# Kernel optimization log

Measured on AMD Instinct MI355X. Metric: run time of the kernel, lower is better.

Reference implementation:

```python
import jax, jax.numpy as jnp
import numpy as np

B, S, F, H, NL, T = 64, 512, 256, 512, 1, 96
HA = H // 8  # attention hidden size (scale_factor=8)


def _p(key, shape, scale=0.05):
    return jax.random.normal(key, shape, dtype=jnp.float32) * scale


def setup_inputs() -> dict:
    key = jax.random.key(0)
    ks = jax.random.split(key, 20)
    return {
        "input_seq": jax.random.normal(ks[0], (B, S, F), dtype=jnp.float32),
        "h0": jax.random.normal(ks[1], (B, H), dtype=jnp.float32),
        "c0": jax.random.normal(ks[2], (B, H), dtype=jnp.float32),
        # encoder LSTM (torch gate order i,f,g,o), combined bias b_ih+b_hh
        "W_ih_e": _p(ks[3], (4 * H, F)),
        "W_hh_e": _p(ks[4], (4 * H, H)),
        "b_e": _p(ks[5], (4 * H,)),
        # decoder LSTM
        "W_ih_d": _p(ks[6], (4 * H, F)),
        "W_hh_d": _p(ks[7], (4 * H, H)),
        "b_d": _p(ks[8], (4 * H,)),
        # attention
        "We_p": _p(ks[9], (HA, H)),
        "be_p": _p(ks[10], (HA,)),
        "Wh_p": _p(ks[11], (HA, H)),
        "bh_p": _p(ks[12], (HA,)),
        "Wa": _p(ks[13], (HA, 2 * HA)),
        "ba": _p(ks[14], (HA,)),
        "v": jax.random.uniform(ks[15], (HA,), dtype=jnp.float32),
        # output linear: (H + HA) -> F
        "Wo": _p(ks[16], (F, H + HA)),
        "bo": _p(ks[17], (F,)),
        "output_size": T,
    }


def _lstm_step(x, h, c, Wih, Whh, b):
    gates = x @ Wih.T + h @ Whh.T + b  # (B, 4H)
    i, f, g, o = jnp.split(gates, 4, axis=-1)
    i, f, o = jax.nn.sigmoid(i), jax.nn.sigmoid(f), jax.nn.sigmoid(o)
    c = f * c + i * jnp.tanh(g)
    h = o * jnp.tanh(c)
    return h, c


def reference(input_seq, h0, c0, W_ih_e, W_hh_e, b_e, W_ih_d, W_hh_d, b_d,
              We_p, be_p, Wh_p, bh_p, Wa, ba, v, Wo, bo, output_size):
    # ---- encoder LSTM over seq (time-major scan) ----
    xs = jnp.swapaxes(input_seq, 0, 1)  # (S, B, F)

    def enc_step(carry, x):
        h, c = carry
        h, c = _lstm_step(x, h, c, W_ih_e, W_hh_e, b_e)
        return (h, c), h

    (h, c), enc_hs = jax.lax.scan(enc_step, (h0, c0), xs)
    enc_out = jnp.swapaxes(enc_hs, 0, 1)  # (B, S, H)

    # encoder projection (same every decode step; hoisted)
    enc_proj = enc_out @ We_p.T + be_p  # (B, S, HA)
    # split attn Linear weight: first HA cols act on hidden, last HA on enc_proj
    Wa_h, Wa_e = Wa[:, :HA], Wa[:, HA:]
    enc_attn = enc_proj @ Wa_e.T  # (B, S, HA)

    def dec_step(carry, _):
        x, h, c = carry
        # Bahdanau attention (uses pre-LSTM hidden h, per original)
        hq = h @ Wh_p.T + bh_p  # (B, HA)
        energy = jnp.tanh(hq[:, None, :] @ Wa_h.T + enc_attn + ba)  # (B, S, HA)
        scores = jnp.einsum('bsh,h->bs', energy, v)
        aw = jax.nn.softmax(scores, axis=1)  # (B, S)
        ctx = jnp.einsum('bs,bsh->bh', aw, enc_proj)  # (B, HA)
        # single-step decoder LSTM
        h, c = _lstm_step(x, h, c, W_ih_d, W_hh_d, b_d)
        out = jnp.concatenate([h, ctx], axis=1) @ Wo.T + bo  # (B, F)
        return (out, h, c), out

    carry0 = (input_seq[:, -1, :], h, c)
    _, preds = jax.lax.scan(dec_step, carry0, None, length=output_size)  # (T, B, F)
    # outputs[:, :, t] = pred_t; return outputs[:, -1, :] -> last feature over time
    return preds[:, :, -1].T  # (B, T)
```

## Files before the change

kernel.cpp:

```cpp
#include <hip/hip_runtime.h>


namespace {

__device__ __forceinline__ float fsigmoid(float x) {
    return 1.0f / (1.0f + __expf(-x));
}
__device__ __forceinline__ float ftanh(float x) {
    float e = __expf(2.0f * x);
    return 1.0f - 2.0f / (e + 1.0f);
}

__device__ __forceinline__ void coh_store(float* p, float v) {
    __hip_atomic_store(p, v, __ATOMIC_RELAXED, __HIP_MEMORY_SCOPE_AGENT);
}
__device__ __forceinline__ void coh_store2(float* p, float2 v) {
    union { float2 f; unsigned long long u; } cv; cv.f = v;
    __hip_atomic_store((unsigned long long*)p, cv.u,
                       __ATOMIC_RELAXED, __HIP_MEMORY_SCOPE_AGENT);
}

__device__ __forceinline__ void post_flag_rep(unsigned* flags, int stride,
                                              int idx, unsigned val) {
    if (threadIdx.x == 0) {
        asm volatile("s_waitcnt vmcnt(0)" ::: "memory");
        #pragma unroll
        for (int r = 0; r < 8; ++r)
            __hip_atomic_store(&flags[r * stride + idx], val,
                               __ATOMIC_RELAXED, __HIP_MEMORY_SCOPE_AGENT);
    }
}
__device__ __forceinline__ void wait_group(const unsigned* flags, int base,
                                           int mask, unsigned val) {
    const unsigned* f = flags + base + (threadIdx.x & mask);
    for (;;) {
        unsigned x = __hip_atomic_load(f, __ATOMIC_RELAXED, __HIP_MEMORY_SCOPE_AGENT);
        if (__all(x >= val)) break;
        __builtin_amdgcn_s_sleep(1);
    }
    asm volatile("" ::: "memory");
}
__device__ __forceinline__ void wait_lstm_inputs(const unsigned* attnF,
                                                 const unsigned* lstmF,
                                                 int w, unsigned val) {
    int lane = threadIdx.x & 63;
    const unsigned* fa = attnF + lane * 2;
    const unsigned* fl = lstmF + (w & 3) * 32 + (lane & 31);
    for (;;) {
        unsigned a = __hip_atomic_load(fa + 0, __ATOMIC_RELAXED, __HIP_MEMORY_SCOPE_AGENT);
        unsigned b = __hip_atomic_load(fa + 1, __ATOMIC_RELAXED, __HIP_MEMORY_SCOPE_AGENT);
        unsigned c = __hip_atomic_load(fl,     __ATOMIC_RELAXED, __HIP_MEMORY_SCOPE_AGENT);
        int ok = (a >= val) && (b >= val) && (c >= val);
        if (__all(ok)) break;
        __builtin_amdgcn_s_sleep(1);
    }
    asm volatile("" ::: "memory");
}

__global__ __launch_bounds__(256) void k_transpose_input(
    const float* __restrict__ in, float4* __restrict__ xQ)
{
    __shared__ float tile[64][65];
    int s  = blockIdx.x >> 2;
    int f0 = (blockIdx.x & 3) * 64;
    int lane = threadIdx.x & 63;
    int r0   = threadIdx.x >> 6;
    for (int r = r0; r < 64; r += 4)
        tile[r][lane] = in[(size_t)r * (512 * 256) + s * 256 + f0 + lane];
    __syncthreads();
    for (int q = r0; q < 16; q += 4) {
        float4 vv = make_float4(tile[lane][4*q], tile[lane][4*q+1],
                                tile[lane][4*q+2], tile[lane][4*q+3]);
        xQ[((size_t)s * 64 + (f0 >> 2) + q) * 64 + lane] = vv;
    }
}

__global__ __launch_bounds__(256) void k_prep(
    const float* __restrict__ We_p, const float* __restrict__ Wh_p,
    const float* __restrict__ h0,   const float* __restrict__ c0,
    const float* __restrict__ Wa,
    float* __restrict__ We_pT, float* __restrict__ Wh_pT,
    float* __restrict__ encH0, float* __restrict__ cT,
    float* __restrict__ WahT,  float* __restrict__ WaeT)
{
    int idx = blockIdx.x * blockDim.x + threadIdx.x;
    const int total = 32768 * 4 + 4096 * 2;
    for (; idx < total; idx += gridDim.x * blockDim.x) {
        if (idx < 32768) {
            int u = idx >> 6, h = idx & 63;
            We_pT[idx] = We_p[h * 512 + u];
        } else if (idx < 65536) {
            int i2 = idx - 32768; int k = i2 >> 6, i = i2 & 63;
            Wh_pT[i2] = Wh_p[i * 512 + k];
        } else if (idx < 98304) {
            int i2 = idx - 65536; int u = i2 >> 6, b = i2 & 63;
            encH0[(u >> 2) * 256 + b * 4 + (u & 3)] = h0[b * 512 + u];
        } else if (idx < 131072) {
            int i2 = idx - 98304; int u = i2 >> 6, b = i2 & 63;
            cT[i2] = c0[b * 512 + u];
        } else if (idx < 135168) {
            int i2 = idx - 131072; int j = i2 >> 6, i = i2 & 63;
            WahT[i2] = Wa[i * 128 + j];
        } else {
            int i2 = idx - 135168; int h2 = i2 >> 6, h = i2 & 63;
            WaeT[i2] = Wa[h * 128 + 64 + h2];
        }
    }
}

__global__ __launch_bounds__(256) void k_prep_wcomb(
    const float* __restrict__ Wih, const float* __restrict__ Whh,
    const float* __restrict__ Wo,  const float* __restrict__ bd,
    const float* __restrict__ bo,
    float* __restrict__ Wh, float* __restrict__ Wc, float* __restrict__ bprime)
{
    int r = blockIdx.x;
    for (int j = threadIdx.x; j < 576; j += 256) {
        float acc = 0.f;
        for (int f = 0; f < 256; ++f)
            acc = fmaf(Wih[r * 256 + f], Wo[f * 576 + j], acc);
        if (j < 512) Wh[(size_t)r * 512 + j] = acc + Whh[(size_t)r * 512 + j];
        else         Wc[(size_t)r * 64 + (j - 512)] = acc;
    }
    if (threadIdx.x == 0) {
        float s = bd[r];
        for (int f = 0; f < 256; ++f)
            s = fmaf(Wih[r * 256 + f], bo[f], s);
        bprime[r] = s;
    }
}

__global__ __launch_bounds__(256) void k_prep_g0(
    const float4* __restrict__ xQlast, const float* __restrict__ Wih,
    const float* __restrict__ bd, float* __restrict__ g0)
{
    int r = blockIdx.x * 4 + ((int)threadIdx.x >> 6);
    int lane = threadIdx.x & 63;
    const float4* Wih4 = (const float4*)Wih;
    float acc = bd[r];
    for (int q = 0; q < 64; ++q) {
        float4 a  = xQlast[q * 64 + lane];
        float4 wv = Wih4[(size_t)r * 64 + q];
        acc = fmaf(a.x, wv.x, acc); acc = fmaf(a.y, wv.y, acc);
        acc = fmaf(a.z, wv.z, acc); acc = fmaf(a.w, wv.w, acc);
    }
    g0[(size_t)r * 64 + lane] = acc;
}

template<int NQ>
__device__ __forceinline__ void accum_seg_pf(
    float acc[8], const float4* __restrict__ actQ, int qb,
    const float4* __restrict__ W4, int wstride, int u0, int lane)
{
    float4 a[NQ];
    #pragma unroll
    for (int q = 0; q < NQ; ++q)
        a[q] = actQ[(qb + q) * 64 + lane];
    #pragma unroll
    for (int q = 0; q < NQ; ++q) {
        #pragma unroll
        for (int uu = 0; uu < 2; ++uu)
            #pragma unroll
            for (int g = 0; g < 4; ++g) {
                float4 wv = W4[(size_t)(g * 512 + u0 + uu) * wstride + (qb + q)];
                float& A = acc[uu * 4 + g];
                A = fmaf(a[q].x, wv.x, A); A = fmaf(a[q].y, wv.y, A);
                A = fmaf(a[q].z, wv.z, A); A = fmaf(a[q].w, wv.w, A);
            }
    }
}

template<int NQ>
__device__ __forceinline__ void accum_seg_pf2(
    float accA[8], float accB[8], const float4* __restrict__ actQ, int qb,
    const float4* __restrict__ W4, int wstride, int u0A, int u0B, int lane)
{
    float4 a[NQ];
    #pragma unroll
    for (int q = 0; q < NQ; ++q)
        a[q] = actQ[(qb + q) * 64 + lane];
    #pragma unroll
    for (int q = 0; q < NQ; ++q) {
        #pragma unroll
        for (int uu = 0; uu < 2; ++uu)
            #pragma unroll
            for (int g = 0; g < 4; ++g) {
                float4 wA = W4[(size_t)(g * 512 + u0A + uu) * wstride + (qb + q)];
                float4 wB = W4[(size_t)(g * 512 + u0B + uu) * wstride + (qb + q)];
                float& A = accA[uu * 4 + g];
                float& Bv = accB[uu * 4 + g];
                A = fmaf(a[q].x, wA.x, A); A = fmaf(a[q].y, wA.y, A);
                A = fmaf(a[q].z, wA.z, A); A = fmaf(a[q].w, wA.w, A);
                Bv = fmaf(a[q].x, wB.x, Bv); Bv = fmaf(a[q].y, wB.y, Bv);
                Bv = fmaf(a[q].z, wB.z, Bv); Bv = fmaf(a[q].w, wB.w, Bv);
            }
    }
}

__device__ __forceinline__ void accum_ctx_reg(
    float acc[8], float4 c0, float4 c1,
    const float4* __restrict__ Wc4, int u0, int w)
{
    #pragma unroll
    for (int uu = 0; uu < 2; ++uu)
        #pragma unroll
        for (int g = 0; g < 4; ++g) {
            float4 w0 = Wc4[(size_t)(g * 512 + u0 + uu) * 16 + w * 2 + 0];
            float4 w1 = Wc4[(size_t)(g * 512 + u0 + uu) * 16 + w * 2 + 1];
            float& A = acc[uu * 4 + g];
            A = fmaf(c0.x, w0.x, A); A = fmaf(c0.y, w0.y, A);
            A = fmaf(c0.z, w0.z, A); A = fmaf(c0.w, w0.w, A);
            A = fmaf(c1.x, w1.x, A); A = fmaf(c1.y, w1.y, A);
            A = fmaf(c1.z, w1.z, A); A = fmaf(c1.w, w1.w, A);
        }
}

__device__ __forceinline__ void lstm_finish_vec(
    int u0, int tid, int w, float acc[8], float2& creg,
    const float* __restrict__ addVec, float* __restrict__ houtSlot, float* smem)
{
    int lane = tid & 63;
    float* part = smem;
    float* gsum = smem + 4096;
    #pragma unroll
    for (int r = 0; r < 8; ++r)
        part[(w * 8 + r) * 64 + lane] = acc[r];
    __syncthreads();
    {
        int b = tid & 63, r = tid >> 6;
        float s = 0.f;
        #pragma unroll
        for (int ww = 0; ww < 8; ++ww)
            s += part[(ww * 8 + r) * 64 + b];
        gsum[r * 64 + b] = s;
    }
    __syncthreads();
    if (tid < 64) {
        int b = tid;
        float cc[2] = {creg.x, creg.y};
        float hv[2];
        #pragma unroll
        for (int uu = 0; uu < 2; ++uu) {
            int u = u0 + uu;
            float gi = gsum[(uu*4+0)*64 + b] + addVec[u];
            float gf = gsum[(uu*4+1)*64 + b] + addVec[512 + u];
            float gg = gsum[(uu*4+2)*64 + b] + addVec[1024 + u];
            float go = gsum[(uu*4+3)*64 + b] + addVec[1536 + u];
            float si = fsigmoid(gi), sf = fsigmoid(gf), so = fsigmoid(go);
            float tg = ftanh(gg);
            float cn = sf * cc[uu] + si * tg;
            cc[uu] = cn;
            hv[uu] = so * ftanh(cn);
        }
        creg = make_float2(cc[0], cc[1]);
        coh_store2(houtSlot + (u0 >> 2) * 256 + b * 4 + (u0 & 3),
                   make_float2(hv[0], hv[1]));
    }
}

template<bool ROWADD>
__device__ __forceinline__ void lstm_finish2(
    int u0A, int u0B, int tid, int w, float accA[8], float accB[8],
    float2& creg, const float* __restrict__ addVec,
    const float* __restrict__ addRowB,
    float* __restrict__ houtSlot, float* smem)
{
    int lane = tid & 63;
    float* part = smem;
    #pragma unroll
    for (int r = 0; r < 8; ++r)
        part[(w * 16 + r) * 64 + lane] = accA[r];
    #pragma unroll
    for (int r = 0; r < 8; ++r)
        part[(w * 16 + 8 + r) * 64 + lane] = accB[r];
    __syncthreads();
    if (tid < 128) {
        int b  = tid & 63;
        int ps = tid >> 6;
        int u0 = ps ? u0B : u0A;
        float cc[2] = {creg.x, creg.y};
        float hv[2];
        #pragma unroll
        for (int uu = 0; uu < 2; ++uu) {
            int u = u0 + uu;
            float gate[4];
            #pragma unroll
            for (int g = 0; g < 4; ++g) {
                int row = ps * 8 + uu * 4 + g;
                float s = 0.f;
                #pragma unroll
                for (int ww = 0; ww < 8; ++ww)
                    s += part[(ww * 16 + row) * 64 + b];
                if (ROWADD) s += addRowB[(size_t)(g * 512 + u) * 64 + b];
                else        s += addVec[g * 512 + u];
                gate[g] = s;
            }
            float si = fsigmoid(gate[0]), sf = fsigmoid(gate[1]);
            float so = fsigmoid(gate[3]);
            float tg = ftanh(gate[2]);
            float cn = sf * cc[uu] + si * tg;
            cc[uu] = cn;
            hv[uu] = so * ftanh(cn);
        }
        creg = make_float2(cc[0], cc[1]);
        coh_store2(houtSlot + (u0 >> 2) * 256 + b * 4 + (u0 & 3),
                   make_float2(hv[0], hv[1]));
        asm volatile("s_waitcnt vmcnt(0)" ::: "memory");
    }
    __syncthreads();
}

__global__ __launch_bounds__(512, 2) void k_enc_persistent(
    const float4* __restrict__ xQ, float* __restrict__ encH,
    float* __restrict__ cT,
    const float* __restrict__ Wih, const float* __restrict__ Whh,
    const float* __restrict__ bias, unsigned* flagsR)
{
    __shared__ float smem[4608];
    int tid = threadIdx.x;
    int lane = tid & 63;
    int w = __builtin_amdgcn_readfirstlane(tid >> 6);
    int bi = blockIdx.x;
    int u0 = bi * 2;
    const unsigned* myFlags = flagsR + (bi & 7) * 256;
    const float4* Wih4 = (const float4*)Wih;
    const float4* Whh4 = (const float4*)Whh;
    float2 creg = make_float2(0.f, 0.f);
    if (tid < 64) { creg.x = cT[u0 * 64 + tid]; creg.y = cT[(u0 + 1) * 64 + tid]; }
    float acc[8];
    #pragma unroll
    for (int r = 0; r < 8; ++r) acc[r] = 0.f;
    accum_seg_pf<8>(acc, xQ, w * 8, Wih4, 64, u0, lane);
    for (int t = 0; t < 512; ++t) {
        wait_group(myFlags, w * 32, 31, (unsigned)t);
        accum_seg_pf<16>(acc, (const float4*)(encH + (size_t)t * 32768),
                         w * 16, Whh4, 128, u0, lane);
        lstm_finish_vec(u0, tid, w, acc, creg, bias,
                        encH + (size_t)(t + 1) * 32768, smem);
        post_flag_rep(flagsR, 256, bi, (unsigned)(t + 1));
        #pragma unroll
        for (int r = 0; r < 8; ++r) acc[r] = 0.f;
        if (t + 1 < 512)
            accum_seg_pf<8>(acc, xQ + (size_t)(t + 1) * 4096, w * 8, Wih4, 64, u0, lane);
    }
    if (tid < 64) { cT[u0 * 64 + tid] = creg.x; cT[(u0 + 1) * 64 + tid] = creg.y; }
}

__global__ __launch_bounds__(256) void k_proj_attn(
    const float* __restrict__ encH,  const float* __restrict__ We_pT,
    const float* __restrict__ be_p,  const float* __restrict__ WaeT,
    const float* __restrict__ ba,
    float* __restrict__ encProj, float* __restrict__ attnPre)
{
    int lane = threadIdx.x & 63;
    int w    = __builtin_amdgcn_readfirstlane((int)threadIdx.x >> 6);
    int wid  = blockIdx.x * 4 + w;
    int b    = wid >> 6;
    int soct = wid & 63;
    float acc[8];
    float bep = be_p[lane];
    #pragma unroll
    for (int j = 0; j < 8; ++j) acc[j] = bep;
    #pragma unroll 2
    for (int q = 0; q < 128; ++q) {
        float w0 = We_pT[(4*q+0) * 64 + lane];
        float w1 = We_pT[(4*q+1) * 64 + lane];
        float w2 = We_pT[(4*q+2) * 64 + lane];
        float w3 = We_pT[(4*q+3) * 64 + lane];
        #pragma unroll
        for (int j = 0; j < 8; ++j) {
            const float4* hb4 = (const float4*)(encH + (size_t)(soct*8 + j + 1) * 32768);
            float4 hv = hb4[q * 64 + b];
            acc[j] = fmaf(hv.x, w0, acc[j]); acc[j] = fmaf(hv.y, w1, acc[j]);
            acc[j] = fmaf(hv.z, w2, acc[j]); acc[j] = fmaf(hv.w, w3, acc[j]);
        }
    }
    #pragma unroll
    for (int j = 0; j < 8; ++j)
        encProj[((size_t)b * 512 + soct * 8 + j) * 64 + lane] = acc[j];
    #pragma unroll
    for (int j = 0; j < 8; ++j) {
        float aa = ba[lane];
        for (int h2 = 0; h2 < 64; ++h2)
            aa = fmaf(__shfl(acc[j], h2), WaeT[h2 * 64 + lane], aa);
        attnPre[((size_t)b * 512 + soct * 8 + j) * 64 + lane] = aa;
    }
}

__global__ __launch_bounds__(256) void k_attn_transpose(
    const float* __restrict__ attnPre, float* __restrict__ attnPreT)
{
    __shared__ float tile[64][65];
    int b  = blockIdx.x >> 3;
    int s0 = (blockIdx.x & 7) * 64;
    int lane = threadIdx.x & 63;
    int r0   = threadIdx.x >> 6;
    for (int r = r0; r < 64; r += 4)
        tile[r][lane] = attnPre[(size_t)b * 32768 + (size_t)(s0 + r) * 64 + lane];
    __syncthreads();
    for (int r = r0; r < 64; r += 4)
        attnPreT[(size_t)b * 32768 + (size_t)r * 512 + s0 + lane] = tile[lane][r];
}

__device__ __forceinline__ void attention_half(
    int b, int tid, int w, int lane,
    const float* __restrict__ hcur,
    const float* __restrict__ Wh_pT, const float* __restrict__ bh_p,
    const float* __restrict__ WahT,  const float* __restrict__ v,
    const float* __restrict__ apL,
    const float* __restrict__ epL,
    float* __restrict__ ctxsumOut,
    float* __restrict__ mSOut,
    float* smem)
{
    float* hq  = smem;
    float* hWa = smem + 64;
    float* sc  = smem + 128;
    float* part = smem + 384;
    float* red  = smem + 896;
    {
        const float4* h4 = (const float4*)hcur;
        float4 hv[16];
        #pragma unroll
        for (int j = 0; j < 16; ++j)
            hv[j] = h4[(w * 16 + j) * 64 + b];
        float p = 0.f;
        #pragma unroll
        for (int j = 0; j < 16; ++j) {
            int q = w * 16 + j;
            p = fmaf(hv[j].x, Wh_pT[(4*q+0) * 64 + lane], p);
            p = fmaf(hv[j].y, Wh_pT[(4*q+1) * 64 + lane], p);
            p = fmaf(hv[j].z, Wh_pT[(4*q+2) * 64 + lane], p);
            p = fmaf(hv[j].w, Wh_pT[(4*q+3) * 64 + lane], p);
        }
        part[w * 64 + lane] = p;
    }
    __syncthreads();
    if (tid < 64) {
        float s = bh_p[tid];
        #pragma unroll
        for (int ww = 0; ww < 8; ++ww) s += part[ww * 64 + tid];
        hq[tid] = s;
    }
    __syncthreads();
    if (tid < 64) {
        float s = 0.f;
        for (int j = 0; j < 64; ++j)
            s = fmaf(hq[j], WahT[j * 64 + tid], s);
        hWa[tid] = s;
    }
    __syncthreads();
    {
        int sp  = tid & 255;
        int hh0 = (tid >> 8) * 32;
        float acc = 0.f;
        for (int j = 0; j < 32; ++j) {
            int h = hh0 + j;
            float e = ftanh(hWa[h] + apL[h * 256 + sp]);
            acc = fmaf(v[h], e, acc);
        }
        part[tid] = acc;
    }
    __syncthreads();
    if (tid < 256)
        sc[tid] = part[tid] + part[256 + tid];
    __syncthreads();
    if (tid < 256) {
        float x = sc[tid];
        float m = x;
        #pragma unroll
        for (int off = 32; off > 0; off >>= 1)
            m = fmaxf(m, __shfl_xor(m, off));
        if (lane == 0) red[w] = m;
    }
    __syncthreads();
    if (tid == 0)
        red[8] = fmaxf(fmaxf(red[0], red[1]), fmaxf(red[2], red[3]));
    __syncthreads();
    float M = red[8];
    if (tid < 256) {
        float e = __expf(sc[tid] - M);
        sc[tid] = e;
        float s = e;
        #pragma unroll
        for (int off = 32; off > 0; off >>= 1)
            s += __shfl_xor(s, off);
        if (lane == 0) red[w] = s;
    }
    __syncthreads();
    if (tid == 0)
        red[9] = ((red[0] + red[1]) + (red[2] + red[3]));
    __syncthreads();
    {
        float a = 0.f;
        for (int i = 0; i < 32; ++i) {
            int sp2 = w * 32 + i;
            a = fmaf(sc[sp2], epL[sp2 * 64 + lane], a);
        }
        part[w * 64 + lane] = a;
    }
    __syncthreads();
    if (tid < 64) {
        float s = 0.f;
        #pragma unroll
        for (int ww = 0; ww < 8; ++ww) s += part[ww * 64 + tid];
        coh_store(&ctxsumOut[(tid >> 2) * 256 + b * 4 + (tid & 3)], s);
    }
    if (tid == 0) {
        coh_store(&mSOut[b], M);
        coh_store(&mSOut[64 + b], red[9]);
    }
    __syncthreads();
}

__device__ __forceinline__ void load_ctx_quads(
    int t, int w, int lane,
    const float* __restrict__ ctxsumH, const float* __restrict__ mSbuf,
    float4& c0, float4& c1)
{
    const float* mS = mSbuf + (size_t)(t - 1) * 256;
    float m0 = mS[lane],       S0 = mS[64 + lane];
    float m1 = mS[128 + lane], S1 = mS[192 + lane];
    float M  = fmaxf(m0, m1);
    float e0 = __expf(m0 - M), e1 = __expf(m1 - M);
    float inv = 1.0f / (e0 * S0 + e1 * S1);
    e0 *= inv; e1 *= inv;
    const float4* a0 = (const float4*)(ctxsumH + (size_t)(t - 1) * 8192);
    const float4* a1 = (const float4*)(ctxsumH + (size_t)(t - 1) * 8192 + 4096);
    float4 x0 = a0[(w * 2 + 0) * 64 + lane];
    float4 y0 = a1[(w * 2 + 0) * 64 + lane];
    float4 x1 = a0[(w * 2 + 1) * 64 + lane];
    float4 y1 = a1[(w * 2 + 1) * 64 + lane];
    c0 = make_float4(e0 * x0.x + e1 * y0.x, e0 * x0.y + e1 * y0.y,
                     e0 * x0.z + e1 * y0.z, e0 * x0.w + e1 * y0.w);
    c1 = make_float4(e0 * x1.x + e1 * y1.x, e0 * x1.y + e1 * y1.y,
                     e0 * x1.z + e1 * y1.z, e0 * x1.w + e1 * y1.w);
}

extern __shared__ float dynsmem[];
__global__ __launch_bounds__(512) void k_dec_persistent(
    const float* __restrict__ encHend,
    float* __restrict__ dechH,
    float* __restrict__ cT,
    const float* __restrict__ Whh,
    const float* __restrict__ Wh,
    const float* __restrict__ Wc,
    const float* __restrict__ g0, const float* __restrict__ bprime,
    const float* __restrict__ Wh_pT, const float* __restrict__ bh_p,
    const float* __restrict__ WahT,  const float* __restrict__ v,
    const float* __restrict__ attnPreT, const float* __restrict__ encProj,
    float* __restrict__ ctxsumH,
    float* __restrict__ mSbuf,
    unsigned* attnFlagsR, unsigned* lstmFlagsR)
{
    float* smem = dynsmem;
    float* apL  = dynsmem + 4608;
    float* epL  = apL + 16384;
    int tid = threadIdx.x;
    int lane = tid & 63;
    int w = __builtin_amdgcn_readfirstlane(tid >> 6);
    int bi = blockIdx.x;
    int rep = bi & 7;
    const unsigned* myLstmF = lstmFlagsR + rep * 128;
    const unsigned* myAttnF = attnFlagsR + rep * 128;
    if (bi < 128) {
        int b = bi & 63, half = bi >> 6;
        {
            const float4* src = (const float4*)(attnPreT + (size_t)b * 32768 + half * 256);
            float4* dst = (float4*)apL;
            for (int i = tid; i < 4096; i += 512) {
                int h = i >> 6, qc = i & 63;
                dst[i] = src[(size_t)h * 128 + qc];
            }
        }
        {
            const float4* src = (const float4*)(encProj + ((size_t)b * 512 + half * 256) * 64);
            float4* dst = (float4*)epL;
            for (int i = tid; i < 4096; i += 512)
                dst[i] = src[i];
        }
        __syncthreads();
        for (int t = 0; t < 96; ++t) {
            if (t) wait_group(myLstmF, (w & 3) * 32, 31, (unsigned)t);
            const float* hc = t ? dechH + (size_t)(t - 1) * 32768 : encHend;
            attention_half(b, tid, w, lane, hc, Wh_pT, bh_p, WahT, v,
                           apL, epL,
                           ctxsumH + (size_t)t * 8192 + half * 4096,
                           mSbuf + (size_t)t * 256 + half * 128, smem);
            post_flag_rep(attnFlagsR, 128, bi, (unsigned)(t + 1));
        }
    } else {
        int u0A = (bi - 128) * 2;
        int u0B = u0A + 256;
        const float4* Whh4 = (const float4*)Whh;
        const float4* Wh4  = (const float4*)Wh;
        const float4* Wc4  = (const float4*)Wc;
        float2 creg = make_float2(0.f, 0.f);
        if (tid < 64) {
            creg.x = cT[u0A * 64 + tid]; creg.y = cT[(u0A + 1) * 64 + tid];
        } else if (tid < 128) {
            creg.x = cT[u0B * 64 + (tid - 64)];
            creg.y = cT[(u0B + 1) * 64 + (tid - 64)];
        }
        for (int t = 0; t < 96; ++t) {
            if (t) wait_lstm_inputs(myAttnF, myLstmF, w, (unsigned)t);
            const float* hc = t ? dechH + (size_t)(t - 1) * 32768 : encHend;
            float* hn = dechH + (size_t)t * 32768;
            float accA[8], accB[8];
            #pragma unroll
            for (int r = 0; r < 8; ++r) { accA[r] = 0.f; accB[r] = 0.f; }
            if (t == 0) {
                accum_seg_pf2<16>(accA, accB, (const float4*)hc, w * 16,
                                  Whh4, 128, u0A, u0B, lane);
                lstm_finish2<true>(u0A, u0B, tid, w, accA, accB, creg,
                                   nullptr, g0, hn, smem);
            } else {
                float4 cq0, cq1;
                load_ctx_quads(t, w, lane, ctxsumH, mSbuf, cq0, cq1);
                accum_seg_pf2<16>(accA, accB, (const float4*)hc, w * 16,
                                  Wh4, 128, u0A, u0B, lane);
                accum_ctx_reg(accA, cq0, cq1, Wc4, u0A, w);
                accum_ctx_reg(accB, cq0, cq1, Wc4, u0B, w);
                lstm_finish2<false>(u0A, u0B, tid, w, accA, accB, creg,
                                    bprime, nullptr, hn, smem);
            }
            post_flag_rep(lstmFlagsR, 128, bi - 128, (unsigned)(t + 1));
        }
    }
}

__global__ __launch_bounds__(256) void k_dout(
    const float* __restrict__ dechH,
    const float* __restrict__ ctxsumH, const float* __restrict__ mSbuf,
    const float* __restrict__ Wo, const float* __restrict__ bo,
    float* __restrict__ dout)
{
    __shared__ float part[256];
    int tau = blockIdx.x;
    int tid = threadIdx.x;
    int lane = tid & 63;
    int w = tid >> 6;
    const float* hq = dechH + (size_t)tau * 32768;
    const float* wrow = Wo + 255 * 576;
    float acc = 0.f;
    for (int i = w * 128; i < w * 128 + 128; ++i)
        acc = fmaf(wrow[i], hq[(i >> 2) * 256 + lane * 4 + (i & 3)], acc);
    part[w * 64 + lane] = acc;
    __syncthreads();
    if (tid < 64) {
        int b = tid;
        const float* mS = mSbuf + (size_t)tau * 256;
        float m0 = mS[b],       S0 = mS[64 + b];
        float m1 = mS[128 + b], S1 = mS[192 + b];
        float M  = fmaxf(m0, m1);
        float e0 = __expf(m0 - M), e1 = __expf(m1 - M);
        float inv = 1.0f / (e0 * S0 + e1 * S1);
        e0 *= inv; e1 *= inv;
        const float* cs0 = ctxsumH + (size_t)tau * 8192;
        const float* cs1 = cs0 + 4096;
        float a2 = bo[255];
        for (int h2 = 0; h2 < 64; ++h2) {
            int idx = (h2 >> 2) * 256 + b * 4 + (h2 & 3);
            a2 = fmaf(wrow[512 + h2], e0 * cs0[idx] + e1 * cs1[idx], a2);
        }
        float s = a2 + part[b] + part[64 + b] + part[128 + b] + part[192 + b];
        dout[b * 96 + tau] = s;
    }
}

}

extern "C" void kernel_launch(void* const* d_in, const int* in_sizes, int n_in,
                              void* d_out, int out_size, void* d_ws, size_t ws_size,
                              hipStream_t stream)
{
    (void)in_sizes; (void)n_in; (void)out_size; (void)ws_size;
    const float* input_seq = (const float*)d_in[0];
    const float* h0     = (const float*)d_in[1];
    const float* c0     = (const float*)d_in[2];
    const float* W_ih_e = (const float*)d_in[3];
    const float* W_hh_e = (const float*)d_in[4];
    const float* b_e    = (const float*)d_in[5];
    const float* W_ih_d = (const float*)d_in[6];
    const float* W_hh_d = (const float*)d_in[7];
    const float* b_d    = (const float*)d_in[8];
    const float* We_p   = (const float*)d_in[9];
    const float* be_p   = (const float*)d_in[10];
    const float* Wh_p   = (const float*)d_in[11];
    const float* bh_p   = (const float*)d_in[12];
    const float* Wa     = (const float*)d_in[13];
    const float* ba     = (const float*)d_in[14];
    const float* v      = (const float*)d_in[15];
    const float* Wo     = (const float*)d_in[16];
    const float* bo     = (const float*)d_in[17];
    float* out = (float*)d_out;

    unsigned* encFlagsR  = (unsigned*)d_ws;
    unsigned* attnFlagsR = encFlagsR + 2048;
    unsigned* lstmFlagsR = attnFlagsR + 1024;
    float* ws       = (float*)d_ws + 4096;
    float* xT       = ws;
    float* encH     = xT + 8388608;
    float* cT       = encH + 16809984;
    float* We_pT    = cT + 32768;
    float* Wh_pT    = We_pT + 32768;
    float* WahT     = Wh_pT + 32768;
    float* WaeT     = WahT + 4096;
    float* encProj  = WaeT + 4096;
    float* attnPre  = encProj + 2097152;
    float* dechH    = attnPre + 2097152;
    float* ctxsumH  = dechH + 3145728;
    float* mSbuf    = ctxsumH + 786432;
    float* Wh       = mSbuf + 24576;
    float* Wc       = Wh + 1048576;
    float* bprime   = Wc + 131072;
    float* g0       = bprime + 2048;
    float* attnPreT = xT;

    (void)hipFuncSetAttribute((const void*)k_dec_persistent,
                              hipFuncAttributeMaxDynamicSharedMemorySize, 149504);

    (void)hipMemsetAsync(d_ws, 0, 16384, stream);
    k_transpose_input<<<2048, 256, 0, stream>>>(input_seq, (float4*)xT);
    k_prep<<<544, 256, 0, stream>>>(We_p, Wh_p, h0, c0, Wa,
                                    We_pT, Wh_pT, encH, cT, WahT, WaeT);
    k_prep_wcomb<<<2048, 256, 0, stream>>>(W_ih_d, W_hh_d, Wo, b_d, bo,
                                           Wh, Wc, bprime);
    k_prep_g0<<<512, 256, 0, stream>>>((const float4*)(xT + (size_t)511 * 16384),
                                       W_ih_d, b_d, g0);
    k_enc_persistent<<<256, 512, 0, stream>>>((const float4*)xT, encH, cT,
                                              W_ih_e, W_hh_e, b_e, encFlagsR);
    k_proj_attn<<<1024, 256, 0, stream>>>(encH, We_pT, be_p, WaeT, ba,
                                          encProj, attnPre);
    k_attn_transpose<<<512, 256, 0, stream>>>(attnPre, attnPreT);
    k_dec_persistent<<<256, 512, 149504, stream>>>(encH + (size_t)512 * 32768,
                                                   dechH, cT,
                                                   W_hh_d, Wh, Wc, g0, bprime,
                                                   Wh_pT, bh_p, WahT, v,
                                                   attnPreT, encProj,
                                                   ctxsumH, mSbuf,
                                                   attnFlagsR, lstmFlagsR);
    k_dout<<<96, 256, 0, stream>>>(dechH, ctxsumH, mSbuf, Wo, bo, out);
}
```

Before: 5.226 ms.

## Replace encoder step flags with sentinel-polled hidden-state data

The encoder's per-step flag wait and flag post are removed. Instead, each wave polls the hidden-state slab directly with atomic loads until the values differ from a sentinel pattern that a new memset writes over the whole encH buffer beforehand. This removes one flag round-trip per timestep and lets each wave start as soon as its own slice is written, rather than waiting for a group of blocks. In exchange it adds a 64 MB memset, polling traffic on the data itself, and relies on a computed value never equalling the sentinel bits.

```diff
diff --git a/kernel.cpp b/kernel.cpp
--- a/kernel.cpp
+++ b/kernel.cpp
@@ -2,6 +2,8 @@
 
 
 namespace {
+
+#define H_SENTINEL 0x7F7F7F7Fu
 
 __device__ __forceinline__ float fsigmoid(float x) {
     return 1.0f / (1.0f + __expf(-x));
@@ -170,6 +172,52 @@
     }
 }
 
+__device__ __forceinline__ void accum_h_poll(
+    float acc[8], const float* __restrict__ hslab, int w,
+    const float4* __restrict__ W4, int u0, int lane)
+{
+    const unsigned long long* hp = (const unsigned long long*)hslab;
+    #pragma unroll
+    for (int jg = 0; jg < 4; ++jg) {
+        unsigned long long uv[8];
+        unsigned pend = 0xFFu;
+        for (;;) {
+            #pragma unroll
+            for (int i = 0; i < 8; ++i) {
+                if (pend & (1u << i)) {
+                    int q = w * 16 + jg * 4 + (i >> 1);
+                    unsigned long long x = __hip_atomic_load(
+                        &hp[(size_t)q * 128 + lane * 2 + (i & 1)],
+                        __ATOMIC_RELAXED, __HIP_MEMORY_SCOPE_AGENT);
+                    if ((unsigned)x != H_SENTINEL) {
+                        uv[i] = x;
+                        pend &= ~(1u << i);
+                    }
+                }
+            }
+            if (__all(pend == 0)) break;
+            __builtin_amdgcn_s_sleep(1);
+        }
+        asm volatile("" ::: "memory");
+        #pragma unroll
+        for (int j = 0; j < 4; ++j) {
+            int q = jg * 4 + j;
+            union { unsigned long long u; float2 f; } lo, hi;
+            lo.u = uv[2 * j]; hi.u = uv[2 * j + 1];
+            float ax = lo.f.x, ay = lo.f.y, az = hi.f.x, aw = hi.f.y;
+            #pragma unroll
+            for (int uu = 0; uu < 2; ++uu)
+                #pragma unroll
+                for (int g = 0; g < 4; ++g) {
+                    float4 wv = W4[(size_t)(g * 512 + u0 + uu) * 128 + (w * 16 + q)];
+                    float& A = acc[uu * 4 + g];
+                    A = fmaf(ax, wv.x, A); A = fmaf(ay, wv.y, A);
+                    A = fmaf(az, wv.z, A); A = fmaf(aw, wv.w, A);
+                }
+        }
+    }
+}
+
 template<int NQ>
 __device__ __forceinline__ void accum_seg_pf2(
     float accA[8], float accB[8], const float4* __restrict__ actQ, int qb,
@@ -314,7 +362,7 @@
     const float4* __restrict__ xQ, float* __restrict__ encH,
     float* __restrict__ cT,
     const float* __restrict__ Wih, const float* __restrict__ Whh,
-    const float* __restrict__ bias, unsigned* flagsR)
+    const float* __restrict__ bias)
 {
     __shared__ float smem[4608];
     int tid = threadIdx.x;
@@ -322,7 +370,6 @@
     int w = __builtin_amdgcn_readfirstlane(tid >> 6);
     int bi = blockIdx.x;
     int u0 = bi * 2;
-    const unsigned* myFlags = flagsR + (bi & 7) * 256;
     const float4* Wih4 = (const float4*)Wih;
     const float4* Whh4 = (const float4*)Whh;
     float2 creg = make_float2(0.f, 0.f);
@@ -332,12 +379,9 @@
     for (int r = 0; r < 8; ++r) acc[r] = 0.f;
     accum_seg_pf<8>(acc, xQ, w * 8, Wih4, 64, u0, lane);
     for (int t = 0; t < 512; ++t) {
-        wait_group(myFlags, w * 32, 31, (unsigned)t);
-        accum_seg_pf<16>(acc, (const float4*)(encH + (size_t)t * 32768),
-                         w * 16, Whh4, 128, u0, lane);
+        accum_h_poll(acc, encH + (size_t)t * 32768, w, Whh4, u0, lane);
         lstm_finish_vec(u0, tid, w, acc, creg, bias,
                         encH + (size_t)(t + 1) * 32768, smem);
-        post_flag_rep(flagsR, 256, bi, (unsigned)(t + 1));
         #pragma unroll
         for (int r = 0; r < 8; ++r) acc[r] = 0.f;
         if (t + 1 < 512)
@@ -695,8 +739,7 @@
     const float* bo     = (const float*)d_in[17];
     float* out = (float*)d_out;
 
-    unsigned* encFlagsR  = (unsigned*)d_ws;
-    unsigned* attnFlagsR = encFlagsR + 2048;
+    unsigned* attnFlagsR = (unsigned*)d_ws;
     unsigned* lstmFlagsR = attnFlagsR + 1024;
     float* ws       = (float*)d_ws + 4096;
     float* xT       = ws;
@@ -721,6 +764,7 @@
                               hipFuncAttributeMaxDynamicSharedMemorySize, 149504);
 
     (void)hipMemsetAsync(d_ws, 0, 16384, stream);
+    (void)hipMemsetAsync(encH + 32768, 0x7F, (size_t)512 * 32768 * 4, stream);
     k_transpose_input<<<2048, 256, 0, stream>>>(input_seq, (float4*)xT);
     k_prep<<<544, 256, 0, stream>>>(We_p, Wh_p, h0, c0, Wa,
                                     We_pT, Wh_pT, encH, cT, WahT, WaeT);
@@ -729,7 +773,7 @@
     k_prep_g0<<<512, 256, 0, stream>>>((const float4*)(xT + (size_t)511 * 16384),
                                        W_ih_d, b_d, g0);
     k_enc_persistent<<<256, 512, 0, stream>>>((const float4*)xT, encH, cT,
-                                              W_ih_e, W_hh_e, b_e, encFlagsR);
+                                              W_ih_e, W_hh_e, b_e);
     k_proj_attn<<<1024, 256, 0, stream>>>(encH, We_pT, be_p, WaeT, ba,
                                           encProj, attnPre);
     k_attn_transpose<<<512, 256, 0, stream>>>(attnPre, attnPreT);
```

Result: slower. 9.361 ms (+79.1%).

## Fold decoder weight-combine and g0 prep into encoder persistent kernel slack

Applied to the files above, without the earlier changes.

Removes the separate k_prep_wcomb and k_prep_g0 launches. Their work is spread across the first 16 timesteps of the persistent encoder kernel: each block computes 8 combined-weight rows and 8 g0 rows, placed after it posts its step flag. This is meant to hide the prep work in the idle time while blocks wait on inter-block flags, and to save two launches. The risk is that the extra work sits on the serial recurrence's critical path in those early steps and delays other blocks waiting on the flags. The g0 path also adds extra __syncthreads and shared-memory scratch use.

```diff
diff --git a/kernel.cpp b/kernel.cpp
--- a/kernel.cpp
+++ b/kernel.cpp
@@ -108,45 +108,6 @@
     }
 }
 
-__global__ __launch_bounds__(256) void k_prep_wcomb(
-    const float* __restrict__ Wih, const float* __restrict__ Whh,
-    const float* __restrict__ Wo,  const float* __restrict__ bd,
-    const float* __restrict__ bo,
-    float* __restrict__ Wh, float* __restrict__ Wc, float* __restrict__ bprime)
-{
-    int r = blockIdx.x;
-    for (int j = threadIdx.x; j < 576; j += 256) {
-        float acc = 0.f;
-        for (int f = 0; f < 256; ++f)
-            acc = fmaf(Wih[r * 256 + f], Wo[f * 576 + j], acc);
-        if (j < 512) Wh[(size_t)r * 512 + j] = acc + Whh[(size_t)r * 512 + j];
-        else         Wc[(size_t)r * 64 + (j - 512)] = acc;
-    }
-    if (threadIdx.x == 0) {
-        float s = bd[r];
-        for (int f = 0; f < 256; ++f)
-            s = fmaf(Wih[r * 256 + f], bo[f], s);
-        bprime[r] = s;
-    }
-}
-
-__global__ __launch_bounds__(256) void k_prep_g0(
-    const float4* __restrict__ xQlast, const float* __restrict__ Wih,
-    const float* __restrict__ bd, float* __restrict__ g0)
-{
-    int r = blockIdx.x * 4 + ((int)threadIdx.x >> 6);
-    int lane = threadIdx.x & 63;
-    const float4* Wih4 = (const float4*)Wih;
-    float acc = bd[r];
-    for (int q = 0; q < 64; ++q) {
-        float4 a  = xQlast[q * 64 + lane];
-        float4 wv = Wih4[(size_t)r * 64 + q];
-        acc = fmaf(a.x, wv.x, acc); acc = fmaf(a.y, wv.y, acc);
-        acc = fmaf(a.z, wv.z, acc); acc = fmaf(a.w, wv.w, acc);
-    }
-    g0[(size_t)r * 64 + lane] = acc;
-}
-
 template<int NQ>
 __device__ __forceinline__ void accum_seg_pf(
     float acc[8], const float4* __restrict__ actQ, int qb,
@@ -310,11 +271,65 @@
     __syncthreads();
 }
 
+__device__ __forceinline__ void wcomb_row(
+    int r, int tid,
+    const float* __restrict__ WihD, const float* __restrict__ WhhD,
+    const float* __restrict__ Wo,   const float* __restrict__ bd,
+    const float* __restrict__ bo,
+    float* __restrict__ Wh, float* __restrict__ Wc, float* __restrict__ bprime)
+{
+    for (int j = tid; j < 576; j += 512) {
+        float acc = 0.f;
+        for (int f = 0; f < 256; ++f)
+            acc = fmaf(WihD[r * 256 + f], Wo[f * 576 + j], acc);
+        if (j < 512) Wh[(size_t)r * 512 + j] = acc + WhhD[(size_t)r * 512 + j];
+        else         Wc[(size_t)r * 64 + (j - 512)] = acc;
+    }
+    if (tid == 0) {
+        float s = bd[r];
+        for (int f = 0; f < 256; ++f)
+            s = fmaf(WihD[r * 256 + f], bo[f], s);
+        bprime[r] = s;
+    }
+}
+
+__device__ __forceinline__ void g0_row(
+    int r, int tid, int w, int lane,
+    const float4* __restrict__ xQlast, const float* __restrict__ WihD,
+    const float* __restrict__ bd, float* __restrict__ g0, float* smem)
+{
+    const float4* Wih4 = (const float4*)WihD;
+    float acc = 0.f;
+    #pragma unroll
+    for (int j = 0; j < 8; ++j) {
+        int q = w * 8 + j;
+        float4 a  = xQlast[q * 64 + lane];
+        float4 wv = Wih4[(size_t)r * 64 + q];
+        acc = fmaf(a.x, wv.x, acc); acc = fmaf(a.y, wv.y, acc);
+        acc = fmaf(a.z, wv.z, acc); acc = fmaf(a.w, wv.w, acc);
+    }
+    float* scratch = smem + 4096;
+    __syncthreads();
+    scratch[w * 64 + lane] = acc;
+    __syncthreads();
+    if (tid < 64) {
+        float s = bd[r];
+        #pragma unroll
+        for (int ww = 0; ww < 8; ++ww) s += scratch[ww * 64 + tid];
+        g0[(size_t)r * 64 + tid] = s;
+    }
+}
+
 __global__ __launch_bounds__(512, 2) void k_enc_persistent(
     const float4* __restrict__ xQ, float* __restrict__ encH,
     float* __restrict__ cT,
     const float* __restrict__ Wih, const float* __restrict__ Whh,
-    const float* __restrict__ bias, unsigned* flagsR)
+    const float* __restrict__ bias, unsigned* flagsR,
+    const float* __restrict__ WihD, const float* __restrict__ WhhD,
+    const float* __restrict__ Wo,   const float* __restrict__ bd,
+    const float* __restrict__ bo,
+    float* __restrict__ Wh, float* __restrict__ Wc,
+    float* __restrict__ bprime, float* __restrict__ g0)
 {
     __shared__ float smem[4608];
     int tid = threadIdx.x;
@@ -325,6 +340,7 @@
     const unsigned* myFlags = flagsR + (bi & 7) * 256;
     const float4* Wih4 = (const float4*)Wih;
     const float4* Whh4 = (const float4*)Whh;
+    const float4* xQlast = xQ + (size_t)511 * 4096;
     float2 creg = make_float2(0.f, 0.f);
     if (tid < 64) { creg.x = cT[u0 * 64 + tid]; creg.y = cT[(u0 + 1) * 64 + tid]; }
     float acc[8];
@@ -338,6 +354,10 @@
         lstm_finish_vec(u0, tid, w, acc, creg, bias,
                         encH + (size_t)(t + 1) * 32768, smem);
         post_flag_rep(flagsR, 256, bi, (unsigned)(t + 1));
+        if (t < 8)
+            wcomb_row(bi * 8 + t, tid, WihD, WhhD, Wo, bd, bo, Wh, Wc, bprime);
+        else if (t < 16)
+            g0_row(bi * 8 + (t - 8), tid, w, lane, xQlast, WihD, bd, g0, smem);
         #pragma unroll
         for (int r = 0; r < 8; ++r) acc[r] = 0.f;
         if (t + 1 < 512)
@@ -724,12 +744,10 @@
     k_transpose_input<<<2048, 256, 0, stream>>>(input_seq, (float4*)xT);
     k_prep<<<544, 256, 0, stream>>>(We_p, Wh_p, h0, c0, Wa,
                                     We_pT, Wh_pT, encH, cT, WahT, WaeT);
-    k_prep_wcomb<<<2048, 256, 0, stream>>>(W_ih_d, W_hh_d, Wo, b_d, bo,
-                                           Wh, Wc, bprime);
-    k_prep_g0<<<512, 256, 0, stream>>>((const float4*)(xT + (size_t)511 * 16384),
-                                       W_ih_d, b_d, g0);
     k_enc_persistent<<<256, 512, 0, stream>>>((const float4*)xT, encH, cT,
-                                              W_ih_e, W_hh_e, b_e, encFlagsR);
+                                              W_ih_e, W_hh_e, b_e, encFlagsR,
+                                              W_ih_d, W_hh_d, Wo, b_d, bo,
+                                              Wh, Wc, bprime, g0);
     k_proj_attn<<<1024, 256, 0, stream>>>(encH, We_pT, be_p, WaeT, ba,
                                           encProj, attnPre);
     k_attn_transpose<<<512, 256, 0, stream>>>(attnPre, attnPreT);
```

New measurement: 5.426 ms. 1.04x slower.
